# Performance work log

Hardware: AMD Instinct MI355X
Metric: run time of the kernel (lower is better)

Reference implementation:

```python
import jax, jax.numpy as jnp
import numpy as np

TEMPERATURE = 8.0  # sqrt(d_head=64)

def setup_inputs() -> dict:
    key = jax.random.key(0)
    kq, kk, kv = jax.random.split(key, 3)
    B, S, D = 4, 4096, 64
    Q = jax.random.normal(kq, (B, S, D), dtype=jnp.float32)
    K = jax.random.normal(kk, (B, S, D), dtype=jnp.float32)
    V = jax.random.normal(kv, (B, S, D), dtype=jnp.float32)
    return {"Q": Q, "K": K, "V": V}

def reference(Q, K, V):
    # attn_scores = Q @ K^T / temperature  -> [B, S, S]
    scores = jnp.einsum('bqd,bkd->bqk', Q, K) / TEMPERATURE
    weights = jax.nn.softmax(scores, axis=-1)
    # NOTE: original module multiplies weights by K (not V) -- faithful to source.
    out = jnp.einsum('bqk,bkd->bqd', weights, K)
    return out
```

## Files before the change

kernel.cpp:

```cpp
#include <hip/hip_runtime.h>
#include <hip/hip_bf16.h>


#define SQ   4096
#define DH   64
#define NB   4
#define QBLK 128
#define KBLK 32

typedef __bf16 bf16x8 __attribute__((ext_vector_type(8)));
typedef float  f32x16 __attribute__((ext_vector_type(16)));
typedef unsigned int u32x4 __attribute__((ext_vector_type(4)));

struct Buf {
  unsigned short Ks[KBLK][72];
  unsigned short Kt[DH][36];
};

__device__ __forceinline__ unsigned short f2bf(float f) {
  return __builtin_bit_cast(unsigned short, (__bf16)f);
}
__device__ __forceinline__ float bf2f(unsigned short u) {
  return __builtin_bit_cast(float, (unsigned int)u << 16);
}

template <int NS, bool FINAL>
__global__ __launch_bounds__(256, 4)
void attn_fwd(const float* __restrict__ Qg, const float* __restrict__ Kg,
              float* __restrict__ Og, unsigned short* __restrict__ Uws,
              float* __restrict__ Lws) {
  __shared__ Buf lds[4];
  const int tid  = threadIdx.x;
  const int lane = tid & 63;
  const int c32  = lane & 31;
  const int h    = lane >> 5;

  constexpr int QT = SQ / QBLK;
  const int split = blockIdx.x / (NB * QT);
  const int rem   = blockIdx.x % (NB * QT);
  const int batch = rem / QT;
  const int qt    = rem % QT;
  const int q0w   = qt * QBLK + (tid >> 6) * 32;
  constexpr int NT = (SQ / NS) / KBLK;

  const float cf = 0.18033688011112042f;
  bf16x8 qf[4];
  {
    const float* qrow = Qg + ((size_t)(batch * SQ + q0w + c32)) * DH + 8 * h;
#pragma unroll
    for (int dc = 0; dc < 4; ++dc) {
      const float4 a = *(const float4*)(qrow + dc * 16);
      const float4 b = *(const float4*)(qrow + dc * 16 + 4);
      bf16x8 t;
      t[0] = (__bf16)(a.x * cf); t[1] = (__bf16)(a.y * cf);
      t[2] = (__bf16)(a.z * cf); t[3] = (__bf16)(a.w * cf);
      t[4] = (__bf16)(b.x * cf); t[5] = (__bf16)(b.y * cf);
      t[6] = (__bf16)(b.z * cf); t[7] = (__bf16)(b.w * cf);
      qf[dc] = t;
    }
  }

  f32x16 acc0 = {};
  f32x16 acc1 = {};
  float l = 0.f;

  const float* kbase =
      Kg + (size_t)batch * SQ * DH + (size_t)split * (SQ / NS) * DH;
  const int row0 = (tid >> 4) * 2;
  const int col0 = (tid & 15) * 4;

  float4 f0, f1;
  auto loadv = [&](int t) {
    const float* p = kbase + ((size_t)t * KBLK + row0) * DH + col0;
    f0 = *(const float4*)(p);
    f1 = *(const float4*)(p + DH);
  };
  auto stage = [&](int b) {
    const ushort4 u0 = make_ushort4(f2bf(f0.x), f2bf(f0.y), f2bf(f0.z), f2bf(f0.w));
    const ushort4 u1 = make_ushort4(f2bf(f1.x), f2bf(f1.y), f2bf(f1.z), f2bf(f1.w));
    *(ushort4*)&lds[b].Ks[row0][col0]     = u0;
    *(ushort4*)&lds[b].Ks[row0 + 1][col0] = u1;
    *(unsigned int*)&lds[b].Kt[col0 + 0][row0] = (unsigned)u0.x | ((unsigned)u1.x << 16);
    *(unsigned int*)&lds[b].Kt[col0 + 1][row0] = (unsigned)u0.y | ((unsigned)u1.y << 16);
    *(unsigned int*)&lds[b].Kt[col0 + 2][row0] = (unsigned)u0.z | ((unsigned)u1.z << 16);
    *(unsigned int*)&lds[b].Kt[col0 + 3][row0] = (unsigned)u0.w | ((unsigned)u1.w << 16);
  };
  auto qkt = [&](int b) {
    f32x16 s = {};
#pragma unroll
    for (int dc = 0; dc < 4; ++dc) {
      bf16x8 kf = *(const bf16x8*)&lds[b].Ks[c32][dc * 16 + 8 * h];
      s = __builtin_amdgcn_mfma_f32_32x32x16_bf16(kf, qf[dc], s, 0, 0, 0);
    }
    return s;
  };
  auto smpv = [&](f32x16 sv, int b) {
    float t0 = 0.f, t1 = 0.f;
#pragma unroll
    for (int r = 0; r < 8; ++r) { sv[r] = exp2f(sv[r]); t0 += sv[r]; }
#pragma unroll
    for (int r = 8; r < 16; ++r) { sv[r] = exp2f(sv[r]); t1 += sv[r]; }
    l += t0 + t1;

    unsigned int dw[8];
#pragma unroll
    for (int d = 0; d < 8; ++d)
      asm("v_cvt_pk_bf16_f32 %0, %1, %2"
          : "=v"(dw[d]) : "v"(sv[2 * d]), "v"(sv[2 * d + 1]));
    asm("v_permlane32_swap_b32 %0, %1" : "+v"(dw[0]), "+v"(dw[2]));
    asm("v_permlane32_swap_b32 %0, %1" : "+v"(dw[1]), "+v"(dw[3]));
    asm("v_permlane32_swap_b32 %0, %1" : "+v"(dw[4]), "+v"(dw[6]));
    asm("v_permlane32_swap_b32 %0, %1" : "+v"(dw[5]), "+v"(dw[7]));
    u32x4 w0 = {dw[0], dw[1], dw[2], dw[3]};
    u32x4 w1 = {dw[4], dw[5], dw[6], dw[7]};
    const bf16x8 pb0 = __builtin_bit_cast(bf16x8, w0);
    const bf16x8 pb1 = __builtin_bit_cast(bf16x8, w1);

    bf16x8 t00 = *(const bf16x8*)&lds[b].Kt[c32][8 * h];
    bf16x8 t01 = *(const bf16x8*)&lds[b].Kt[c32][16 + 8 * h];
    bf16x8 t10 = *(const bf16x8*)&lds[b].Kt[32 + c32][8 * h];
    bf16x8 t11 = *(const bf16x8*)&lds[b].Kt[32 + c32][16 + 8 * h];
    acc0 = __builtin_amdgcn_mfma_f32_32x32x16_bf16(t00, pb0, acc0, 0, 0, 0);
    acc0 = __builtin_amdgcn_mfma_f32_32x32x16_bf16(t01, pb1, acc0, 0, 0, 0);
    acc1 = __builtin_amdgcn_mfma_f32_32x32x16_bf16(t10, pb0, acc1, 0, 0, 0);
    acc1 = __builtin_amdgcn_mfma_f32_32x32x16_bf16(t11, pb1, acc1, 0, 0, 0);
  };

  loadv(0); stage(0);
  loadv(1); stage(1);
  loadv(2);
  __syncthreads();
  f32x16 s = qkt(0);

  for (int t = 0; t < NT - 1; ++t) {
    if (t + 2 < NT) stage((t + 2) & 3);
    if (t + 3 < NT) loadv(t + 3);
    __syncthreads();
    f32x16 n = qkt((t + 1) & 3);
    smpv(s, t & 3);
    s = n;
  }
  smpv(s, (NT - 1) & 3);

  l += __shfl_xor(l, 32);

  if (FINAL) {
    const float scale = 1.0f / l;
    float* orow = Og + ((size_t)(batch * SQ) + q0w + c32) * DH;
#pragma unroll
    for (int mm = 0; mm < 4; ++mm) {
      float4 w0 = make_float4(acc0[4 * mm] * scale, acc0[4 * mm + 1] * scale,
                              acc0[4 * mm + 2] * scale, acc0[4 * mm + 3] * scale);
      float4 w1 = make_float4(acc1[4 * mm] * scale, acc1[4 * mm + 1] * scale,
                              acc1[4 * mm + 2] * scale, acc1[4 * mm + 3] * scale);
      *(float4*)(orow + 8 * mm + 4 * h)      = w0;
      *(float4*)(orow + 32 + 8 * mm + 4 * h) = w1;
    }
  } else {
    unsigned short* urow =
        Uws + ((size_t)((split * NB + batch) * SQ) + q0w + c32) * DH;
#pragma unroll
    for (int mm = 0; mm < 4; ++mm) {
      *(ushort4*)(urow + 8 * mm + 4 * h) =
          make_ushort4(f2bf(acc0[4 * mm]), f2bf(acc0[4 * mm + 1]),
                       f2bf(acc0[4 * mm + 2]), f2bf(acc0[4 * mm + 3]));
      *(ushort4*)(urow + 32 + 8 * mm + 4 * h) =
          make_ushort4(f2bf(acc1[4 * mm]), f2bf(acc1[4 * mm + 1]),
                       f2bf(acc1[4 * mm + 2]), f2bf(acc1[4 * mm + 3]));
    }
    if (h == 0)
      Lws[(size_t)(split * NB + batch) * SQ + q0w + c32] = l;
  }
}

template <int NS>
__global__ __launch_bounds__(256, 4)
void combine_splits(const unsigned short* __restrict__ U,
                    const float* __restrict__ L, float* __restrict__ O) {
  const int idx = blockIdx.x * 256 + threadIdx.x;
  const int row = idx >> 4;
  const int d4  = (idx & 15) << 2;
  const int RT  = NB * SQ;

  float den = 0.f;
#pragma unroll
  for (int i = 0; i < NS; ++i) den += L[(size_t)i * RT + row];
  const float rden = 1.0f / den;

  float4 o = make_float4(0.f, 0.f, 0.f, 0.f);
#pragma unroll
  for (int i = 0; i < NS; ++i) {
    const ushort4 u = *(const ushort4*)&U[((size_t)i * RT + row) * DH + d4];
    o.x += bf2f(u.x); o.y += bf2f(u.y); o.z += bf2f(u.z); o.w += bf2f(u.w);
  }
  o.x *= rden; o.y *= rden; o.z *= rden; o.w *= rden;
  *(float4*)&O[(size_t)row * DH + d4] = o;
}

extern "C" void kernel_launch(void* const* d_in, const int* in_sizes, int n_in,
                              void* d_out, int out_size, void* d_ws, size_t ws_size,
                              hipStream_t stream) {
  const float* Q = (const float*)d_in[0];
  const float* K = (const float*)d_in[1];
  float* O = (float*)d_out;

  auto need = [](int ns) {
    return (size_t)ns * NB * SQ * DH * 2 + (size_t)ns * NB * SQ * 4;
  };

  if (ws_size >= need(8)) {
    constexpr int NS = 8;
    unsigned short* U = (unsigned short*)d_ws;
    float* L = (float*)(U + (size_t)NS * NB * SQ * DH);
    attn_fwd<NS, false><<<dim3(NS * NB * (SQ / QBLK)), 256, 0, stream>>>(Q, K, nullptr, U, L);
    combine_splits<NS><<<dim3((NB * SQ * 16) / 256), 256, 0, stream>>>(U, L, O);
  } else if (ws_size >= need(4)) {
    constexpr int NS = 4;
    unsigned short* U = (unsigned short*)d_ws;
    float* L = (float*)(U + (size_t)NS * NB * SQ * DH);
    attn_fwd<NS, false><<<dim3(NS * NB * (SQ / QBLK)), 256, 0, stream>>>(Q, K, nullptr, U, L);
    combine_splits<NS><<<dim3((NB * SQ * 16) / 256), 256, 0, stream>>>(U, L, O);
  } else {
    attn_fwd<1, true><<<dim3(NB * (SQ / QBLK)), 256, 0, stream>>>(Q, K, O, nullptr, nullptr);
  }
}
```

Measured before the change: 43.74 us.

## Precompute swizzled bf16 K tiles and stream them via direct global-to-LDS loads

Adds a pre-pass kernel that converts K to bf16 once per call, in both row and transposed layouts with an XOR swizzle, and writes a per-tile image. The attention kernel then fills LDS with global_load_lds DMA instead of per-block fp32 loads, conversion and scattered transposed stores. Barriers become explicit vmcnt waits. The padded LDS layout is replaced by swizzled addressing to avoid bank conflicts. This removes redundant per-block conversion and transpose work and frees registers, at the cost of an extra kernel launch and a workspace round trip. The fallback path also places the image in the workspace without checking its size.

```diff
diff --git a/kernel.cpp b/kernel.cpp
--- a/kernel.cpp
+++ b/kernel.cpp
@@ -7,14 +7,16 @@
 #define NB   4
 #define QBLK 128
 #define KBLK 32
+#define NTILES (SQ / KBLK)
 
 typedef __bf16 bf16x8 __attribute__((ext_vector_type(8)));
 typedef float  f32x16 __attribute__((ext_vector_type(16)));
 typedef unsigned int u32x4 __attribute__((ext_vector_type(4)));
+typedef unsigned short u16x8 __attribute__((ext_vector_type(8)));
 
 struct Buf {
-  unsigned short Ks[KBLK][72];
-  unsigned short Kt[DH][36];
+  unsigned short Ks[KBLK][64];
+  unsigned short Kt[DH][32];
 };
 
 __device__ __forceinline__ unsigned short f2bf(float f) {
@@ -23,14 +25,58 @@
 __device__ __forceinline__ float bf2f(unsigned short u) {
   return __builtin_bit_cast(float, (unsigned int)u << 16);
 }
+__device__ __forceinline__ void gload16(const void* g, void* l) {
+  __builtin_amdgcn_global_load_lds(
+      (const __attribute__((address_space(1))) void*)g,
+      (__attribute__((address_space(3))) void*)l, 16, 0, 0);
+}
+
+__global__ __launch_bounds__(256, 4)
+void conv_img(const float* __restrict__ K, unsigned short* __restrict__ img) {
+  __shared__ float tile[KBLK][DH + 1];
+  const int b   = blockIdx.x / NTILES;
+  const int t   = blockIdx.x % NTILES;
+  const int tid = threadIdx.x;
+  {
+    const float* src = K + ((size_t)b * SQ + t * KBLK) * DH;
+    const int r = tid >> 3, c = (tid & 7) * 8;
+    const float4 a = *(const float4*)(src + r * DH + c);
+    const float4 d = *(const float4*)(src + r * DH + c + 4);
+    tile[r][c + 0] = a.x; tile[r][c + 1] = a.y;
+    tile[r][c + 2] = a.z; tile[r][c + 3] = a.w;
+    tile[r][c + 4] = d.x; tile[r][c + 5] = d.y;
+    tile[r][c + 6] = d.z; tile[r][c + 7] = d.w;
+  }
+  __syncthreads();
+  unsigned short* out = img + ((size_t)b * NTILES + t) * 4096;
+#pragma unroll
+  for (int cc = 0; cc < 2; ++cc) {
+    const int ck = tid * 2 + cc;
+    u16x8 v;
+    if (ck < 256) {
+      const int row = ck >> 3;
+      const int d0  = ((ck & 7) ^ (row & 7)) << 3;
+#pragma unroll
+      for (int i = 0; i < 8; ++i) v[i] = f2bf(tile[row][d0 + i]);
+    } else {
+      const int ck2 = ck - 256;
+      const int d   = ck2 >> 2;
+      const int k0  = ((ck2 & 3) ^ (d & 3)) << 3;
+#pragma unroll
+      for (int i = 0; i < 8; ++i) v[i] = f2bf(tile[k0 + i][d]);
+    }
+    *(u16x8*)(out + ck * 8) = v;
+  }
+}
 
 template <int NS, bool FINAL>
 __global__ __launch_bounds__(256, 4)
-void attn_fwd(const float* __restrict__ Qg, const float* __restrict__ Kg,
+void attn_fwd(const float* __restrict__ Qg, const unsigned short* __restrict__ img,
               float* __restrict__ Og, unsigned short* __restrict__ Uws,
               float* __restrict__ Lws) {
   __shared__ Buf lds[4];
   const int tid  = threadIdx.x;
+  const int wave = tid >> 6;
   const int lane = tid & 63;
   const int c32  = lane & 31;
   const int h    = lane >> 5;
@@ -40,7 +86,7 @@
   const int rem   = blockIdx.x % (NB * QT);
   const int batch = rem / QT;
   const int qt    = rem % QT;
-  const int q0w   = qt * QBLK + (tid >> 6) * 32;
+  const int q0w   = qt * QBLK + wave * 32;
   constexpr int NT = (SQ / NS) / KBLK;
 
   const float cf = 0.18033688011112042f;
@@ -64,32 +110,21 @@
   f32x16 acc1 = {};
   float l = 0.f;
 
-  const float* kbase =
-      Kg + (size_t)batch * SQ * DH + (size_t)split * (SQ / NS) * DH;
-  const int row0 = (tid >> 4) * 2;
-  const int col0 = (tid & 15) * 4;
-
-  float4 f0, f1;
-  auto loadv = [&](int t) {
-    const float* p = kbase + ((size_t)t * KBLK + row0) * DH + col0;
-    f0 = *(const float4*)(p);
-    f1 = *(const float4*)(p + DH);
-  };
-  auto stage = [&](int b) {
-    const ushort4 u0 = make_ushort4(f2bf(f0.x), f2bf(f0.y), f2bf(f0.z), f2bf(f0.w));
-    const ushort4 u1 = make_ushort4(f2bf(f1.x), f2bf(f1.y), f2bf(f1.z), f2bf(f1.w));
-    *(ushort4*)&lds[b].Ks[row0][col0]     = u0;
-    *(ushort4*)&lds[b].Ks[row0 + 1][col0] = u1;
-    *(unsigned int*)&lds[b].Kt[col0 + 0][row0] = (unsigned)u0.x | ((unsigned)u1.x << 16);
-    *(unsigned int*)&lds[b].Kt[col0 + 1][row0] = (unsigned)u0.y | ((unsigned)u1.y << 16);
-    *(unsigned int*)&lds[b].Kt[col0 + 2][row0] = (unsigned)u0.z | ((unsigned)u1.z << 16);
-    *(unsigned int*)&lds[b].Kt[col0 + 3][row0] = (unsigned)u0.w | ((unsigned)u1.w << 16);
-  };
+  const int tile0 = (split * (SQ / NS)) / KBLK;
+  const unsigned short* ibase = img + ((size_t)batch * NTILES + tile0) * 4096;
+
+  auto issue = [&](int t, int b) {
+    const unsigned short* g = ibase + (size_t)t * 4096 + wave * 512 + lane * 8;
+    char* lb = (char*)&lds[b] + wave * 1024;
+    gload16(g, lb);
+    gload16(g + 2048, lb + 4096);
+  };
+
   auto qkt = [&](int b) {
     f32x16 s = {};
 #pragma unroll
     for (int dc = 0; dc < 4; ++dc) {
-      bf16x8 kf = *(const bf16x8*)&lds[b].Ks[c32][dc * 16 + 8 * h];
+      bf16x8 kf = *(const bf16x8*)&lds[b].Ks[c32][(((2 * dc + h) ^ (c32 & 7)) << 3)];
       s = __builtin_amdgcn_mfma_f32_32x32x16_bf16(kf, qf[dc], s, 0, 0, 0);
     }
     return s;
@@ -116,26 +151,33 @@
     const bf16x8 pb0 = __builtin_bit_cast(bf16x8, w0);
     const bf16x8 pb1 = __builtin_bit_cast(bf16x8, w1);
 
-    bf16x8 t00 = *(const bf16x8*)&lds[b].Kt[c32][8 * h];
-    bf16x8 t01 = *(const bf16x8*)&lds[b].Kt[c32][16 + 8 * h];
-    bf16x8 t10 = *(const bf16x8*)&lds[b].Kt[32 + c32][8 * h];
-    bf16x8 t11 = *(const bf16x8*)&lds[b].Kt[32 + c32][16 + 8 * h];
-    acc0 = __builtin_amdgcn_mfma_f32_32x32x16_bf16(t00, pb0, acc0, 0, 0, 0);
-    acc0 = __builtin_amdgcn_mfma_f32_32x32x16_bf16(t01, pb1, acc0, 0, 0, 0);
-    acc1 = __builtin_amdgcn_mfma_f32_32x32x16_bf16(t10, pb0, acc1, 0, 0, 0);
-    acc1 = __builtin_amdgcn_mfma_f32_32x32x16_bf16(t11, pb1, acc1, 0, 0, 0);
-  };
-
-  loadv(0); stage(0);
-  loadv(1); stage(1);
-  loadv(2);
-  __syncthreads();
+    const int x3 = c32 & 3;
+    bf16x8 tf0 = *(const bf16x8*)&lds[b].Kt[c32][((h ^ x3) << 3)];
+    bf16x8 tf1 = *(const bf16x8*)&lds[b].Kt[c32][(((2 + h) ^ x3) << 3)];
+    bf16x8 tf2 = *(const bf16x8*)&lds[b].Kt[32 + c32][((h ^ x3) << 3)];
+    bf16x8 tf3 = *(const bf16x8*)&lds[b].Kt[32 + c32][(((2 + h) ^ x3) << 3)];
+    acc0 = __builtin_amdgcn_mfma_f32_32x32x16_bf16(tf0, pb0, acc0, 0, 0, 0);
+    acc0 = __builtin_amdgcn_mfma_f32_32x32x16_bf16(tf1, pb1, acc0, 0, 0, 0);
+    acc1 = __builtin_amdgcn_mfma_f32_32x32x16_bf16(tf2, pb0, acc1, 0, 0, 0);
+    acc1 = __builtin_amdgcn_mfma_f32_32x32x16_bf16(tf3, pb1, acc1, 0, 0, 0);
+  };
+
+  issue(0, 0);
+  issue(1, 1);
+  asm volatile("s_waitcnt vmcnt(2)" ::: "memory");
+  __builtin_amdgcn_s_barrier();
+  __builtin_amdgcn_sched_barrier(0);
   f32x16 s = qkt(0);
 
   for (int t = 0; t < NT - 1; ++t) {
-    if (t + 2 < NT) stage((t + 2) & 3);
-    if (t + 3 < NT) loadv(t + 3);
-    __syncthreads();
+    if (t + 2 < NT) {
+      issue(t + 2, (t + 2) & 3);
+      asm volatile("s_waitcnt vmcnt(2)" ::: "memory");
+    } else {
+      asm volatile("s_waitcnt vmcnt(0)" ::: "memory");
+    }
+    __builtin_amdgcn_s_barrier();
+    __builtin_amdgcn_sched_barrier(0);
     f32x16 n = qkt((t + 1) & 3);
     smpv(s, t & 3);
     s = n;
@@ -204,23 +246,30 @@
   const float* K = (const float*)d_in[1];
   float* O = (float*)d_out;
 
-  auto need = [](int ns) {
-    return (size_t)ns * NB * SQ * DH * 2 + (size_t)ns * NB * SQ * 4;
+  const size_t imgElems = (size_t)NB * NTILES * 4096;
+  auto need = [&](int ns) {
+    return (size_t)ns * NB * SQ * DH * 2 + (size_t)ns * NB * SQ * 4 + imgElems * 2;
   };
 
   if (ws_size >= need(8)) {
     constexpr int NS = 8;
     unsigned short* U = (unsigned short*)d_ws;
     float* L = (float*)(U + (size_t)NS * NB * SQ * DH);
-    attn_fwd<NS, false><<<dim3(NS * NB * (SQ / QBLK)), 256, 0, stream>>>(Q, K, nullptr, U, L);
+    unsigned short* img = (unsigned short*)(L + (size_t)NS * NB * SQ);
+    conv_img<<<dim3(NB * NTILES), 256, 0, stream>>>(K, img);
+    attn_fwd<NS, false><<<dim3(NS * NB * (SQ / QBLK)), 256, 0, stream>>>(Q, img, nullptr, U, L);
     combine_splits<NS><<<dim3((NB * SQ * 16) / 256), 256, 0, stream>>>(U, L, O);
   } else if (ws_size >= need(4)) {
     constexpr int NS = 4;
     unsigned short* U = (unsigned short*)d_ws;
     float* L = (float*)(U + (size_t)NS * NB * SQ * DH);
-    attn_fwd<NS, false><<<dim3(NS * NB * (SQ / QBLK)), 256, 0, stream>>>(Q, K, nullptr, U, L);
+    unsigned short* img = (unsigned short*)(L + (size_t)NS * NB * SQ);
+    conv_img<<<dim3(NB * NTILES), 256, 0, stream>>>(K, img);
+    attn_fwd<NS, false><<<dim3(NS * NB * (SQ / QBLK)), 256, 0, stream>>>(Q, img, nullptr, U, L);
     combine_splits<NS><<<dim3((NB * SQ * 16) / 256), 256, 0, stream>>>(U, L, O);
   } else {
-    attn_fwd<1, true><<<dim3(NB * (SQ / QBLK)), 256, 0, stream>>>(Q, K, O, nullptr, nullptr);
-  }
-}
+    unsigned short* img = (unsigned short*)d_ws;
+    conv_img<<<dim3(NB * NTILES), 256, 0, stream>>>(K, img);
+    attn_fwd<1, true><<<dim3(NB * (SQ / QBLK)), 256, 0, stream>>>(Q, img, O, nullptr, nullptr);
+  }
+}
```

New measurement: 45.48 us. 4.0% more time.
